# Performance work log

Measured on AMD Instinct MI355X. Metric: run time of the kernel, lower is better.

The kernel has to match this reference:

```python
import jax, jax.numpy as jnp
import numpy as np

B = 2048
IN = 1024
M = 256
P = M * (M + 1) // 2  # 32896 Cholesky params


def setup_inputs() -> dict:
    key = jax.random.key(0)
    k1, k2, k3 = jax.random.split(key, 3)
    x = jax.random.normal(k1, (B, IN), dtype=jnp.float32)
    # nn.Linear(input_size, P): weight [P, IN], bias [P]
    bound = 1.0 / np.sqrt(IN)
    W = jax.random.uniform(k2, (P, IN), dtype=jnp.float32, minval=-bound, maxval=bound)
    b = jax.random.uniform(k3, (P,), dtype=jnp.float32, minval=-bound, maxval=bound)
    return {"x": x, "W": W, "b": b}


def reference(x, W, b):
    # Linear projection to packed lower-triangular params [B, P]
    chol_params = x @ W.T + b
    # Row-major lower-triangular fill order matches the torch double loop:
    # (0,0),(1,0),(1,1),(2,0),...
    rows, cols = jnp.tril_indices(M)
    diag_mask = rows == cols  # [P]
    vals = jnp.where(diag_mask[None, :], jax.nn.relu(chol_params), chol_params)
    L = jnp.zeros((x.shape[0], M, M), dtype=chol_params.dtype)
    L = L.at[:, rows, cols].set(vals)
    # Batched L @ L^T -> positive semi-definite matrix [B, M, M]
    return jnp.einsum('bik,bjk->bij', L, L)
```

## Files before the change

kernel.cpp:

```cpp
#include <hip/hip_runtime.h>

#define B_DIM 2048
#define IN_DIM 1024
#define M_DIM 256
#define P_DIM 32896
#define RTP_B 40960
#define CRTP_BYTES (167772160)
#define WQ_BYTES   (33685504)
#define XQ_BYTES   (2097152)

typedef __attribute__((ext_vector_type(4)))  int   i32x4;
typedef __attribute__((ext_vector_type(4)))  float f32x4;
typedef __attribute__((ext_vector_type(8)))  short short8;

#define GLD16(gsrc, ldst) __builtin_amdgcn_global_load_lds(                    \
    (const __attribute__((address_space(1))) unsigned int*)(gsrc),             \
    (__attribute__((address_space(3))) unsigned int*)(ldst), 16, 0, 0)

__device__ __forceinline__ unsigned short f2bf(float f) {
    unsigned int u = __float_as_uint(f);
    u += 0x7FFFu + ((u >> 16) & 1u);
    return (unsigned short)(u >> 16);
}
__device__ __forceinline__ int rtp0(int r) {
    const int g = r >> 6;
    return 2048 * g * (g + 1) + (r & 63) * ((g + 1) << 6);
}
__device__ __forceinline__ int rtp_off(int r, int c) {
    return rtp0(r) + (((c >> 3) ^ (r & 7)) << 3) + (c & 7);
}

#define NW_BLK 8224
#define NX_BLK 512
#define NZ_BLK 2048
__global__ void prep_all(const float* __restrict__ X, const float* __restrict__ W,
                         signed char* __restrict__ Xq, signed char* __restrict__ Wq,
                         float* __restrict__ Sx, unsigned short* __restrict__ Crtp) {
    const int bid = blockIdx.x, tid = threadIdx.x;
    if (bid < NW_BLK) {
#pragma unroll
        for (int u = 0; u < 4; ++u) {
            const int i = bid * 1024 + u * 256 + tid;
            float4 v = reinterpret_cast<const float4*>(W)[i];
            const int q0 = (int)rintf(v.x * 4064.f), q1 = (int)rintf(v.y * 4064.f);
            const int q2 = (int)rintf(v.z * 4064.f), q3 = (int)rintf(v.w * 4064.f);
            reinterpret_cast<unsigned int*>(Wq)[i] =
                (q0 & 255) | ((q1 & 255) << 8) | ((q2 & 255) << 16) | ((unsigned)(q3 & 255) << 24);
        }
    } else if (bid < NW_BLK + NX_BLK) {
        const int wv  = tid >> 6, ln = tid & 63;
        const int row = (bid - NW_BLK) * 4 + wv;
        const float* xr = X + (size_t)row * IN_DIM + ln * 16;
        float f[16];
#pragma unroll
        for (int u = 0; u < 4; ++u) {
            float4 v = reinterpret_cast<const float4*>(xr)[u];
            f[u * 4 + 0] = v.x; f[u * 4 + 1] = v.y; f[u * 4 + 2] = v.z; f[u * 4 + 3] = v.w;
        }
        float m = 0.f;
#pragma unroll
        for (int e = 0; e < 16; ++e) m = fmaxf(m, fabsf(f[e]));
#pragma unroll
        for (int off = 1; off < 64; off <<= 1) m = fmaxf(m, __shfl_xor(m, off));
        const float inv = m > 1e-30f ? 127.f / m : 0.f;
        unsigned int w4[4];
#pragma unroll
        for (int u = 0; u < 4; ++u) {
            const int q0 = (int)rintf(f[u * 4 + 0] * inv), q1 = (int)rintf(f[u * 4 + 1] * inv);
            const int q2 = (int)rintf(f[u * 4 + 2] * inv), q3 = (int)rintf(f[u * 4 + 3] * inv);
            w4[u] = (q0 & 255) | ((q1 & 255) << 8) | ((q2 & 255) << 16) | ((unsigned)(q3 & 255) << 24);
        }
        reinterpret_cast<uint4*>(Xq + (size_t)row * IN_DIM)[ln] =
            make_uint4(w4[0], w4[1], w4[2], w4[3]);
        if (ln == 0) Sx[row] = m / (127.f * 4064.f);
    } else {
        const int b = bid - NW_BLK - NX_BLK;
        const int r = tid;
        const int g = r >> 6;
        const int nch = (g + 1) << 3;
        const int xm = r & 7;
        unsigned short* base = Crtp + (size_t)b * RTP_B + rtp0(r);
        const int pc = (r >> 3) ^ xm;
        for (int c = r + 1; (c >> 3) == (r >> 3); ++c) base[(pc << 3) + (c & 7)] = 0;
        const uint4 z = make_uint4(0u, 0u, 0u, 0u);
        for (int cc = (r >> 3) + 1; cc < nch; ++cc)
            *reinterpret_cast<uint4*>(&base[(cc ^ xm) << 3]) = z;
    }
}

__global__ __launch_bounds__(512) void gemm1_kernel(
    const signed char* __restrict__ Xq, const signed char* __restrict__ Wq,
    const float* __restrict__ bias, const float* __restrict__ Sx,
    unsigned short* __restrict__ Crtp)
{
    __shared__ __align__(16) unsigned char lds[3 * 24576];

    const int lin = blockIdx.x;
    const int x   = lin & 7;
    const int j   = lin >> 3;
    const int rtile = ((x & 1) << 2) + (j & 3);
    const int panel = (x >> 1) * 65 + (j >> 2);
    if (panel >= 257) return;
    const int row0 = rtile << 8;
    const int col0 = panel << 7;

    const int tid  = threadIdx.x;
    const int lane = tid & 63;
    const int wid  = tid >> 6;
    const int wr   = wid >> 1;
    const int wc   = wid & 1;
    const int lr16 = lane & 15;
    const int kq   = lane >> 4;

    const int srow = lane >> 2;
    const int sch  = lane & 3;
    const signed char* gA = Xq + (size_t)(row0 + (wid << 5) + srow) * IN_DIM + (sch << 4);
    const signed char* gB = Wq + (size_t)(col0 + (wid << 4) + srow) * IN_DIM + (sch << 4);

#define STAGE(kt, bufo)                                                          \
    {                                                                            \
        GLD16(gA + ((kt) << 6),                        &lds[(bufo) + (wid << 11)]); \
        GLD16(gA + (size_t)16 * IN_DIM + ((kt) << 6),  &lds[(bufo) + (wid << 11) + 1024]); \
        GLD16(gB + ((kt) << 6),                        &lds[(bufo) + 16384 + (wid << 10)]); \
    }

    i32x4 acc[4][4];
#pragma unroll
    for (int m = 0; m < 4; ++m)
#pragma unroll
        for (int n = 0; n < 4; ++n) acc[m][n] = (i32x4){0, 0, 0, 0};

    int o0 = 0, o1 = 24576, o2 = 49152;
    STAGE(0, o0);
    STAGE(1, o1);

    for (int it = 0; it < 16; ++it) {
        if (it < 15) asm volatile("s_waitcnt vmcnt(3)" ::: "memory");
        else         asm volatile("s_waitcnt vmcnt(0)" ::: "memory");
        __builtin_amdgcn_s_barrier();
        asm volatile("" ::: "memory");

        const int cb = o0;
        i32x4 av[4], bv[4];
#pragma unroll
        for (int m = 0; m < 4; ++m) {
            const int r = (wr << 6) + (m << 4) + lr16;
            av[m] = *reinterpret_cast<const i32x4*>(&lds[cb + (r << 6) + (kq << 4)]);
        }
#pragma unroll
        for (int n = 0; n < 4; ++n) {
            const int r = (wc << 6) + (n << 4) + lr16;
            bv[n] = *reinterpret_cast<const i32x4*>(&lds[cb + 16384 + (r << 6) + (kq << 4)]);
        }
        if (it < 14) STAGE(it + 2, o2);
        __builtin_amdgcn_s_setprio(1);
#pragma unroll
        for (int m = 0; m < 4; ++m)
#pragma unroll
            for (int n = 0; n < 4; ++n)
                acc[m][n] = __builtin_amdgcn_mfma_i32_16x16x64_i8(av[m], bv[n], acc[m][n], 0, 0, 0);
        __builtin_amdgcn_s_setprio(0);

        const int t = o0; o0 = o1; o1 = o2; o2 = t;
    }
#undef STAGE

    float sc[4][4];
#pragma unroll
    for (int m = 0; m < 4; ++m)
#pragma unroll
        for (int q = 0; q < 4; ++q)
            sc[m][q] = Sx[row0 + (wr << 6) + (m << 4) + (kq << 2) + q];

#pragma unroll
    for (int n = 0; n < 4; ++n) {
        const int p = col0 + (wc << 6) + (n << 4) + lr16;
        const float t = sqrtf((float)(8 * p + 1));
        const int rt = (int)((t - 1.0f) * 0.5f + 0.001f);
        const int ct = p - ((rt * (rt + 1)) >> 1);
        const int off = rtp_off(rt, ct);
        const bool diag = (ct == rt);
        const float bvs = bias[p];
#pragma unroll
        for (int m = 0; m < 4; ++m) {
#pragma unroll
            for (int q = 0; q < 4; ++q) {
                const int brow = row0 + (wr << 6) + (m << 4) + (kq << 2) + q;
                float v = (float)acc[m][n][q] * sc[m][q] + bvs;
                if (diag) v = fmaxf(v, 0.f);
                Crtp[(size_t)brow * RTP_B + off] = f2bf(v);
            }
        }
    }
}

__global__ __launch_bounds__(256) void syrk_kernel(
    const unsigned short* __restrict__ Crtp, float* __restrict__ O)
{
    __shared__ unsigned short Lt[RTP_B];
    const int tid  = threadIdx.x;
    const int lane = tid & 63;
    const int wid  = tid >> 6;
    const int b    = blockIdx.x;
    const unsigned short* Cb = Crtp + (size_t)b * RTP_B;

#pragma unroll
    for (int i = 0; i < 20; ++i) {
        const int g = wid * 20 + i;
        GLD16(Cb + g * 512 + (lane << 3), &Lt[g * 512]);
    }
    __syncthreads();

    const int lr16 = lane & 15;
    const int kc   = lane >> 4;
    float* Ob = O + (size_t)b * (M_DIM * M_DIM);

    const unsigned char LIST[4][5] = {
        {0x33, 0x22, 0x00, 0x00, 0x00},
        {0x23, 0x32, 0x01, 0x10, 0x00},
        {0x11, 0x12, 0x21, 0x02, 0x00},
        {0x13, 0x31, 0x03, 0x30, 0x20}};
    const int CNT[4] = {3, 4, 4, 5};
    const int cnt = CNT[wid];

    for (int tt = 0; tt < cnt; ++tt) {
        const int code = LIST[wid][tt];
        const int ti = code >> 4, tj = code & 15;

        int baseA[4], xA[4], baseB[4], xB[4];
#pragma unroll
        for (int m = 0; m < 4; ++m) {
            const int ia = (ti << 6) + (m << 4) + lr16;
            const int jb = (tj << 6) + (m << 4) + lr16;
            baseA[m] = rtp0(ia); xA[m] = ia & 7;
            baseB[m] = rtp0(jb); xB[m] = jb & 7;
        }
        f32x4 acc[4][4];
#pragma unroll
        for (int m = 0; m < 4; ++m)
#pragma unroll
            for (int n = 0; n < 4; ++n) acc[m][n] = (f32x4){0.f, 0.f, 0.f, 0.f};

        const int kmax = ti < tj ? ti : tj;
        for (int kt = 0; kt <= kmax; ++kt) {
#pragma unroll
            for (int s = 0; s < 2; ++s) {
                const int cidx = (kt << 3) + (s << 2) + kc;
                short8 a[4], bb[4];
#pragma unroll
                for (int m = 0; m < 4; ++m)
                    a[m] = *reinterpret_cast<const short8*>(&Lt[baseA[m] + ((cidx ^ xA[m]) << 3)]);
#pragma unroll
                for (int n = 0; n < 4; ++n)
                    bb[n] = *reinterpret_cast<const short8*>(&Lt[baseB[n] + ((cidx ^ xB[n]) << 3)]);
#pragma unroll
                for (int m = 0; m < 4; ++m)
#pragma unroll
                    for (int n = 0; n < 4; ++n)
                        acc[m][n] = __builtin_amdgcn_mfma_f32_16x16x32_bf16(a[m], bb[n], acc[m][n], 0, 0, 0);
            }
        }
#pragma unroll
        for (int m = 0; m < 4; ++m) {
            const int i0 = (ti << 6) + (m << 4) + (kc << 2);
#pragma unroll
            for (int n = 0; n < 4; ++n) {
                const int j = (tj << 6) + (n << 4) + lr16;
#pragma unroll
                for (int q = 0; q < 4; ++q)
                    __builtin_nontemporal_store(acc[m][n][q], &Ob[(size_t)(i0 + q) * M_DIM + j]);
            }
        }
    }
}

extern "C" void kernel_launch(void* const* d_in, const int* in_sizes, int n_in,
                              void* d_out, int out_size, void* d_ws, size_t ws_size,
                              hipStream_t stream)
{
    (void)in_sizes; (void)n_in; (void)out_size; (void)ws_size;
    const float* x    = (const float*)d_in[0];
    const float* W    = (const float*)d_in[1];
    const float* bias = (const float*)d_in[2];
    float* O = (float*)d_out;

    char* ws = (char*)d_ws;
    unsigned short* Crtp = (unsigned short*)ws;
    signed char*    Wq   = (signed char*)(ws + CRTP_BYTES);
    signed char*    Xq   = (signed char*)(ws + CRTP_BYTES + WQ_BYTES);
    float*          Sx   = (float*)(ws + CRTP_BYTES + WQ_BYTES + XQ_BYTES);

    prep_all<<<dim3(NW_BLK + NX_BLK + NZ_BLK), dim3(256), 0, stream>>>(
        x, W, Xq, Wq, Sx, Crtp);
    gemm1_kernel<<<dim3(2080), dim3(512), 0, stream>>>(Xq, Wq, bias, Sx, Crtp);
    syrk_kernel<<<dim3(B_DIM), dim3(256), 0, stream>>>(Crtp, O);
}
```

Before: 334.4 us.

## Halve gemm1 block to 4 waves with 128x64 warp tiles and swizzled LDS

Restructures the int8 GEMM so each block uses 256 threads (4 waves), each wave computing a 128x64 output tile with 8x4 MFMA accumulators instead of 64x64. Each wave now issues six global-to-LDS loads per stage. An XOR swizzle on the 16-byte chunk index is applied to both the LDS writes and the reads to reduce bank conflicts. The larger per-wave tile raises register use, and launch bounds now request 2 blocks per CU. This trades parallelism per block for more MFMA reuse per LDS read.

```diff
diff --git a/kernel.cpp b/kernel.cpp
--- a/kernel.cpp
+++ b/kernel.cpp
@@ -88,7 +88,7 @@
     }
 }
 
-__global__ __launch_bounds__(512) void gemm1_kernel(
+__global__ __launch_bounds__(256, 2) void gemm1_kernel(
     const signed char* __restrict__ Xq, const signed char* __restrict__ Wq,
     const float* __restrict__ bias, const float* __restrict__ Sx,
     unsigned short* __restrict__ Crtp)
@@ -108,25 +108,39 @@
     const int lane = tid & 63;
     const int wid  = tid >> 6;
     const int wr   = wid >> 1;
-    const int wc   = wid & 1;
+    const int wn   = wid & 1;
     const int lr16 = lane & 15;
     const int kq   = lane >> 4;
 
     const int srow = lane >> 2;
-    const int sch  = lane & 3;
-    const signed char* gA = Xq + (size_t)(row0 + (wid << 5) + srow) * IN_DIM + (sch << 4);
-    const signed char* gB = Wq + (size_t)(col0 + (wid << 4) + srow) * IN_DIM + (sch << 4);
-
-#define STAGE(kt, bufo)                                                          \
-    {                                                                            \
-        GLD16(gA + ((kt) << 6),                        &lds[(bufo) + (wid << 11)]); \
-        GLD16(gA + (size_t)16 * IN_DIM + ((kt) << 6),  &lds[(bufo) + (wid << 11) + 1024]); \
-        GLD16(gB + ((kt) << 6),                        &lds[(bufo) + 16384 + (wid << 10)]); \
-    }
-
-    i32x4 acc[4][4];
-#pragma unroll
-    for (int m = 0; m < 4; ++m)
+    const signed char* gsA[4];
+    const signed char* gsB[2];
+#pragma unroll
+    for (int i = 0; i < 4; ++i) {
+        const int ra = (wid << 6) + (i << 4) + srow;
+        const int ch = (lane & 3) ^ ((ra >> 1) & 3);
+        gsA[i] = Xq + (size_t)(row0 + ra) * IN_DIM + (ch << 4);
+    }
+#pragma unroll
+    for (int i = 0; i < 2; ++i) {
+        const int rb = (wid << 5) + (i << 4) + srow;
+        const int ch = (lane & 3) ^ ((rb >> 1) & 3);
+        gsB[i] = Wq + (size_t)(col0 + rb) * IN_DIM + (ch << 4);
+    }
+
+#define STAGE(kt, bufo)                                                            \
+    {                                                                              \
+        GLD16(gsA[0] + ((kt) << 6), &lds[(bufo) + (wid << 12)]);                   \
+        GLD16(gsA[1] + ((kt) << 6), &lds[(bufo) + (wid << 12) + 1024]);            \
+        GLD16(gsA[2] + ((kt) << 6), &lds[(bufo) + (wid << 12) + 2048]);            \
+        GLD16(gsA[3] + ((kt) << 6), &lds[(bufo) + (wid << 12) + 3072]);            \
+        GLD16(gsB[0] + ((kt) << 6), &lds[(bufo) + 16384 + (wid << 11)]);           \
+        GLD16(gsB[1] + ((kt) << 6), &lds[(bufo) + 16384 + (wid << 11) + 1024]);    \
+    }
+
+    i32x4 acc[8][4];
+#pragma unroll
+    for (int m = 0; m < 8; ++m)
 #pragma unroll
         for (int n = 0; n < 4; ++n) acc[m][n] = (i32x4){0, 0, 0, 0};
 
@@ -135,27 +149,29 @@
     STAGE(1, o1);
 
     for (int it = 0; it < 16; ++it) {
-        if (it < 15) asm volatile("s_waitcnt vmcnt(3)" ::: "memory");
+        if (it < 15) asm volatile("s_waitcnt vmcnt(6)" ::: "memory");
         else         asm volatile("s_waitcnt vmcnt(0)" ::: "memory");
         __builtin_amdgcn_s_barrier();
         asm volatile("" ::: "memory");
 
         const int cb = o0;
-        i32x4 av[4], bv[4];
-#pragma unroll
-        for (int m = 0; m < 4; ++m) {
-            const int r = (wr << 6) + (m << 4) + lr16;
-            av[m] = *reinterpret_cast<const i32x4*>(&lds[cb + (r << 6) + (kq << 4)]);
+        i32x4 av[8], bv[4];
+#pragma unroll
+        for (int m = 0; m < 8; ++m) {
+            const int r = (wr << 7) + (m << 4) + lr16;
+            av[m] = *reinterpret_cast<const i32x4*>(
+                &lds[cb + (r << 6) + ((kq ^ ((r >> 1) & 3)) << 4)]);
         }
 #pragma unroll
         for (int n = 0; n < 4; ++n) {
-            const int r = (wc << 6) + (n << 4) + lr16;
-            bv[n] = *reinterpret_cast<const i32x4*>(&lds[cb + 16384 + (r << 6) + (kq << 4)]);
+            const int r = (wn << 6) + (n << 4) + lr16;
+            bv[n] = *reinterpret_cast<const i32x4*>(
+                &lds[cb + 16384 + (r << 6) + ((kq ^ ((r >> 1) & 3)) << 4)]);
         }
         if (it < 14) STAGE(it + 2, o2);
         __builtin_amdgcn_s_setprio(1);
 #pragma unroll
-        for (int m = 0; m < 4; ++m)
+        for (int m = 0; m < 8; ++m)
 #pragma unroll
             for (int n = 0; n < 4; ++n)
                 acc[m][n] = __builtin_amdgcn_mfma_i32_16x16x64_i8(av[m], bv[n], acc[m][n], 0, 0, 0);
@@ -165,16 +181,16 @@
     }
 #undef STAGE
 
-    float sc[4][4];
-#pragma unroll
-    for (int m = 0; m < 4; ++m)
+    float sc[8][4];
+#pragma unroll
+    for (int m = 0; m < 8; ++m)
 #pragma unroll
         for (int q = 0; q < 4; ++q)
-            sc[m][q] = Sx[row0 + (wr << 6) + (m << 4) + (kq << 2) + q];
+            sc[m][q] = Sx[row0 + (wr << 7) + (m << 4) + (kq << 2) + q];
 
 #pragma unroll
     for (int n = 0; n < 4; ++n) {
-        const int p = col0 + (wc << 6) + (n << 4) + lr16;
+        const int p = col0 + (wn << 6) + (n << 4) + lr16;
         const float t = sqrtf((float)(8 * p + 1));
         const int rt = (int)((t - 1.0f) * 0.5f + 0.001f);
         const int ct = p - ((rt * (rt + 1)) >> 1);
@@ -182,10 +198,10 @@
         const bool diag = (ct == rt);
         const float bvs = bias[p];
 #pragma unroll
-        for (int m = 0; m < 4; ++m) {
+        for (int m = 0; m < 8; ++m) {
 #pragma unroll
             for (int q = 0; q < 4; ++q) {
-                const int brow = row0 + (wr << 6) + (m << 4) + (kq << 2) + q;
+                const int brow = row0 + (wr << 7) + (m << 4) + (kq << 2) + q;
                 float v = (float)acc[m][n][q] * sc[m][q] + bvs;
                 if (diag) v = fmaxf(v, 0.f);
                 Crtp[(size_t)brow * RTP_B + off] = f2bf(v);
@@ -292,6 +308,6 @@
 
     prep_all<<<dim3(NW_BLK + NX_BLK + NZ_BLK), dim3(256), 0, stream>>>(
         x, W, Xq, Wq, Sx, Crtp);
-    gemm1_kernel<<<dim3(2080), dim3(512), 0, stream>>>(Xq, Wq, bias, Sx, Crtp);
+    gemm1_kernel<<<dim3(2080), dim3(256), 0, stream>>>(Xq, Wq, bias, Sx, Crtp);
     syrk_kernel<<<dim3(B_DIM), dim3(256), 0, stream>>>(Crtp, O);
 }
```

Result: slower. 349.4 us (+4.5%).

## Exploit output symmetry in SYRK and split tiles across eight waves

Applied to the files above, without the earlier changes.

The SYRK kernel now computes only lower-triangle 64x64 tiles, each split into two 32-row halves. It writes each off-diagonal result to both (i,j) and the transposed (j,i) position instead of recomputing the upper tiles. The block grows to 512 threads (8 waves) with a rebalanced work list to improve load balance and occupancy. The transposed stores are strided, non-coalesced and not nontemporal, which may raise write cost.

```diff
diff --git a/kernel.cpp b/kernel.cpp
--- a/kernel.cpp
+++ b/kernel.cpp
@@ -194,7 +194,7 @@
     }
 }
 
-__global__ __launch_bounds__(256) void syrk_kernel(
+__global__ __launch_bounds__(512) void syrk_kernel(
     const unsigned short* __restrict__ Crtp, float* __restrict__ O)
 {
     __shared__ unsigned short Lt[RTP_B];
@@ -205,8 +205,8 @@
     const unsigned short* Cb = Crtp + (size_t)b * RTP_B;
 
 #pragma unroll
-    for (int i = 0; i < 20; ++i) {
-        const int g = wid * 20 + i;
+    for (int i = 0; i < 10; ++i) {
+        const int g = wid * 10 + i;
         GLD16(Cb + g * 512 + (lane << 3), &Lt[g * 512]);
     }
     __syncthreads();
@@ -215,29 +215,37 @@
     const int kc   = lane >> 4;
     float* Ob = O + (size_t)b * (M_DIM * M_DIM);
 
-    const unsigned char LIST[4][5] = {
-        {0x33, 0x22, 0x00, 0x00, 0x00},
-        {0x23, 0x32, 0x01, 0x10, 0x00},
-        {0x11, 0x12, 0x21, 0x02, 0x00},
-        {0x13, 0x31, 0x03, 0x30, 0x20}};
-    const int CNT[4] = {3, 4, 4, 5};
+    const unsigned char LIST[8][4] = {
+        {0x36, 0x00, 0x00, 0x00},
+        {0x37, 0x01, 0x00, 0x00},
+        {0x34, 0x12, 0x00, 0x00},
+        {0x35, 0x13, 0x00, 0x00},
+        {0x24, 0x22, 0x00, 0x00},
+        {0x25, 0x23, 0x00, 0x00},
+        {0x32, 0x10, 0x20, 0x30},
+        {0x33, 0x11, 0x21, 0x31}};
+    const int CNT[8] = {2, 2, 2, 2, 2, 2, 4, 4};
     const int cnt = CNT[wid];
 
     for (int tt = 0; tt < cnt; ++tt) {
-        const int code = LIST[wid][tt];
-        const int ti = code >> 4, tj = code & 15;
-
-        int baseA[4], xA[4], baseB[4], xB[4];
-#pragma unroll
-        for (int m = 0; m < 4; ++m) {
-            const int ia = (ti << 6) + (m << 4) + lr16;
-            const int jb = (tj << 6) + (m << 4) + lr16;
+        const int c  = LIST[wid][tt];
+        const int ti = c >> 4, tj = (c >> 1) & 7, mh = c & 1;
+        const int ib = (ti << 6) + (mh << 5);
+
+        int baseA[2], xA[2], baseB[4], xB[4];
+#pragma unroll
+        for (int m = 0; m < 2; ++m) {
+            const int ia = ib + (m << 4) + lr16;
             baseA[m] = rtp0(ia); xA[m] = ia & 7;
-            baseB[m] = rtp0(jb); xB[m] = jb & 7;
-        }
-        f32x4 acc[4][4];
-#pragma unroll
-        for (int m = 0; m < 4; ++m)
+        }
+#pragma unroll
+        for (int n = 0; n < 4; ++n) {
+            const int jb = (tj << 6) + (n << 4) + lr16;
+            baseB[n] = rtp0(jb); xB[n] = jb & 7;
+        }
+        f32x4 acc[2][4];
+#pragma unroll
+        for (int m = 0; m < 2; ++m)
 #pragma unroll
             for (int n = 0; n < 4; ++n) acc[m][n] = (f32x4){0.f, 0.f, 0.f, 0.f};
 
@@ -246,29 +254,42 @@
 #pragma unroll
             for (int s = 0; s < 2; ++s) {
                 const int cidx = (kt << 3) + (s << 2) + kc;
-                short8 a[4], bb[4];
-#pragma unroll
-                for (int m = 0; m < 4; ++m)
+                short8 a[2], bb[4];
+#pragma unroll
+                for (int m = 0; m < 2; ++m)
                     a[m] = *reinterpret_cast<const short8*>(&Lt[baseA[m] + ((cidx ^ xA[m]) << 3)]);
 #pragma unroll
                 for (int n = 0; n < 4; ++n)
                     bb[n] = *reinterpret_cast<const short8*>(&Lt[baseB[n] + ((cidx ^ xB[n]) << 3)]);
 #pragma unroll
-                for (int m = 0; m < 4; ++m)
+                for (int m = 0; m < 2; ++m)
 #pragma unroll
                     for (int n = 0; n < 4; ++n)
                         acc[m][n] = __builtin_amdgcn_mfma_f32_16x16x32_bf16(a[m], bb[n], acc[m][n], 0, 0, 0);
             }
         }
 #pragma unroll
-        for (int m = 0; m < 4; ++m) {
-            const int i0 = (ti << 6) + (m << 4) + (kc << 2);
+        for (int m = 0; m < 2; ++m) {
+            const int i0 = ib + (m << 4) + (kc << 2);
 #pragma unroll
             for (int n = 0; n < 4; ++n) {
-                const int j = (tj << 6) + (n << 4) + lr16;
+                const int jj = (tj << 6) + (n << 4) + lr16;
 #pragma unroll
                 for (int q = 0; q < 4; ++q)
-                    __builtin_nontemporal_store(acc[m][n][q], &Ob[(size_t)(i0 + q) * M_DIM + j]);
+                    __builtin_nontemporal_store(acc[m][n][q], &Ob[(size_t)(i0 + q) * M_DIM + jj]);
+            }
+        }
+        if (ti != tj) {
+#pragma unroll
+            for (int m = 0; m < 2; ++m) {
+                const int i0 = ib + (m << 4) + (kc << 2);
+#pragma unroll
+                for (int n = 0; n < 4; ++n) {
+                    const int jj = (tj << 6) + (n << 4) + lr16;
+#pragma unroll
+                    for (int q = 0; q < 4; ++q)
+                        Ob[(size_t)jj * M_DIM + i0 + q] = acc[m][n][q];
+                }
             }
         }
     }
@@ -293,5 +314,5 @@
     prep_all<<<dim3(NW_BLK + NX_BLK + NZ_BLK), dim3(256), 0, stream>>>(
         x, W, Xq, Wq, Sx, Crtp);
     gemm1_kernel<<<dim3(2080), dim3(512), 0, stream>>>(Xq, Wq, bias, Sx, Crtp);
-    syrk_kernel<<<dim3(B_DIM), dim3(256), 0, stream>>>(Crtp, O);
-}
+    syrk_kernel<<<dim3(B_DIM), dim3(512), 0, stream>>>(Crtp, O);
+}
```

After: 345.1 us. 3.2% more time.
